# Optimization experiments

Hardware: AMD Instinct MI355X
Metric: run time of the kernel (lower is better)

The kernel has to match this reference:

```python
import jax, jax.numpy as jnp
import numpy as np

L, N, EMB, H = 4, 50000, 128, 4
R, HID, LBL = 16, 64, 32
E = 625000


def setup_inputs() -> dict:
    key = jax.random.key(0)
    ks = jax.random.split(key, 10)
    s = 0.05
    return {
        "embedding": jax.random.normal(ks[0], (L, N, EMB), jnp.float32),
        "in_proj_w": jax.random.normal(ks[1], (3 * EMB, EMB), jnp.float32) * s,
        "in_proj_b": jnp.zeros((3 * EMB,), jnp.float32),
        "out_proj_w": jax.random.normal(ks[2], (EMB, EMB), jnp.float32) * s,
        "out_proj_b": jnp.zeros((EMB,), jnp.float32),
        "w1": jax.random.normal(ks[3], (R, EMB, HID), jnp.float32) * s,
        "root1": jax.random.normal(ks[4], (EMB, HID), jnp.float32) * s,
        "b1": jnp.zeros((HID,), jnp.float32),
        "w2": jax.random.normal(ks[5], (R, HID, LBL), jnp.float32) * s,
        "root2": jax.random.normal(ks[6], (HID, LBL), jnp.float32) * s,
        "b2": jnp.zeros((LBL,), jnp.float32),
        "edge_index": jax.random.randint(ks[7], (2, E), 0, N, dtype=jnp.int64),
        "edge_type": jax.random.randint(ks[8], (E,), 0, R, dtype=jnp.int64),
    }


def mha_self(x, wi, bi, wo, bo):
    # x: (L, N, EMB) -- torch nn.MultiheadAttention, batch_first=False, q=k=v=x
    Ls, Ns, Es = x.shape
    hd = Es // H
    qkv = x @ wi.T + bi                      # (L, N, 3E)
    q, k, v = jnp.split(qkv, 3, axis=-1)
    q = q.reshape(Ls, Ns, H, hd)
    k = k.reshape(Ls, Ns, H, hd)
    v = v.reshape(Ls, Ns, H, hd)
    scores = jnp.einsum('lnhd,mnhd->nhlm', q, k) / np.sqrt(hd).astype(np.float32)
    attn = jax.nn.softmax(scores, axis=-1)
    out = jnp.einsum('nhlm,mnhd->lnhd', attn, v).reshape(Ls, Ns, Es)
    return out @ wo.T + bo


def rgcn_layer(x, src, dst, etype, W, root, bias):
    # PyG RGCNConv (num_bases=None, aggr='mean'):
    # out[n] = x[n] @ root + bias + sum_r mean_{e: dst=n, type=r} x[src_e] @ W[r]
    Rr, fin, fout = W.shape
    seg = etype * N + dst                                   # (E,) combined (rel, dst)
    msg_sum = jax.ops.segment_sum(x[src], seg, num_segments=Rr * N)   # (R*N, fin)
    cnt = jax.ops.segment_sum(jnp.ones((src.shape[0],), x.dtype), seg,
                              num_segments=Rr * N)
    mean = (msg_sum / jnp.maximum(cnt, 1.0)[:, None]).reshape(Rr, N, fin)
    agg = jnp.einsum('rni,rio->no', mean, W)                # per-relation GEMM
    return agg + x @ root + bias


def reference(embedding, in_proj_w, in_proj_b, out_proj_w, out_proj_b,
              w1, root1, b1, w2, root2, b2, edge_index, edge_type):
    attn_out = mha_self(embedding, in_proj_w, in_proj_b, out_proj_w, out_proj_b)
    x = attn_out[0]                                         # (N, EMB)
    src, dst = edge_index[0], edge_index[1]
    x = jax.nn.relu(rgcn_layer(x, src, dst, edge_type, w1, root1, b1))
    x = rgcn_layer(x, src, dst, edge_type, w2, root2, b2)
    return jax.nn.softmax(x, axis=-1)
```

## Files before the change

### kernel.cpp

```cpp
#include <hip/hip_runtime.h>
#include <hip/hip_bf16.h>
#include <math.h>

#define NNODES 50000
#define NEDGE 625000
#define RREL 16
#define SCAN_NB 196

typedef __attribute__((ext_vector_type(8))) short short8;
typedef __attribute__((ext_vector_type(4))) float f32x4;

__device__ __forceinline__ float bfu(ushort u) {
  return __uint_as_float(((unsigned)u) << 16);
}
__device__ __forceinline__ ushort f2b(float f) {
  __hip_bfloat16 h = __float2bfloat16(f);
  return *(ushort*)&h;
}

__global__ __launch_bounds__(256) void prep_weights(
    const float* __restrict__ ipw, const float* __restrict__ opw,
    const float* __restrict__ w1, const float* __restrict__ root1,
    const float* __restrict__ w2, const float* __restrict__ root2,
    __hip_bfloat16* __restrict__ BTqkv, __hip_bfloat16* __restrict__ BToutT,
    __hip_bfloat16* __restrict__ BT1, __hip_bfloat16* __restrict__ BT2) {
  int i = blockIdx.x * 256 + threadIdx.x;
  if (i < 49152) {
    BTqkv[i] = __float2bfloat16(ipw[i]);
  } else if (i < 65536) {
    int j = i - 49152; int m = j / 128, c = j % 128;
    BToutT[j] = __float2bfloat16(opw[c * 128 + m]);
  } else if (i < 65536 + 139264) {
    int j = i - 65536; int c = j / 128, k = j % 128;
    float v;
    if (c < 64) v = root1[k * 64 + c];
    else { int r = (c - 64) >> 6, o = (c - 64) & 63; v = w1[r * 8192 + k * 64 + o]; }
    BT1[j] = __float2bfloat16(v);
  } else if (i < 65536 + 139264 + 34816) {
    int j = i - 65536 - 139264; int c = j / 64, k = j % 64;
    float v;
    if (c < 32) v = root2[k * 32 + c];
    else { int r = (c - 32) >> 5, o = (c - 32) & 31; v = w2[r * 2048 + k * 32 + o]; }
    BT2[j] = __float2bfloat16(v);
  }
}

__global__ __launch_bounds__(256) void prep_bias1(
    const float* __restrict__ opb, const float* __restrict__ w1,
    const float* __restrict__ root1, float* __restrict__ bias1) {
  int j = blockIdx.x * 256 + threadIdx.x;
  if (j >= 1088) return;
  float s = 0.f;
  if (j < 64) {
    for (int c = 0; c < 128; c++) s += opb[c] * root1[c * 64 + j];
  } else {
    int r = (j - 64) >> 6, o = (j - 64) & 63;
    for (int c = 0; c < 128; c++) s += opb[c] * w1[r * 8192 + c * 64 + o];
  }
  bias1[j] = s;
}

__global__ __launch_bounds__(256) void attn_mega(
    const float* __restrict__ emb, const __hip_bfloat16* __restrict__ BTqkv,
    const float* __restrict__ ipb, __hip_bfloat16* __restrict__ o0) {
  __shared__ ushort Ks[128 * 132];
  __shared__ ushort Vs[128 * 132];
  __shared__ ushort Qs[32 * 132];
  const ushort* BT = (const ushort*)BTqkv;
  const int t = threadIdx.x;
  const int w = t >> 6, lane = t & 63;
  const int lrow = lane & 15, lk = lane >> 4;
  const long nb = (long)blockIdx.x * 32;

  short8 af[2][4];
#pragma unroll
  for (int i = 0; i < 2; i++) {
    long n = nb + 16 * i + lrow;
    if (n > NNODES - 1) n = NNODES - 1;
    const float* ap = emb + ((long)w * NNODES + n) * 128;
#pragma unroll
    for (int k0 = 0; k0 < 4; k0++) {
      float4 f0 = *(const float4*)(ap + k0 * 32 + lk * 8);
      float4 f1 = *(const float4*)(ap + k0 * 32 + lk * 8 + 4);
      int4 v;
      v.x = (int)f2b(f0.x) | ((int)f2b(f0.y) << 16);
      v.y = (int)f2b(f0.z) | ((int)f2b(f0.w) << 16);
      v.z = (int)f2b(f1.x) | ((int)f2b(f1.y) << 16);
      v.w = (int)f2b(f1.z) | ((int)f2b(f1.w) << 16);
      af[i][k0] = *(short8*)&v;
    }
  }

  const float alpha = 0.17677669529663687f;

  if (w == 0) {
#pragma unroll
    for (int half = 0; half < 2; half++) {
      f32x4 acc[2][4];
#pragma unroll
      for (int i = 0; i < 2; i++)
#pragma unroll
        for (int j = 0; j < 4; j++) acc[i][j] = (f32x4){0.f, 0.f, 0.f, 0.f};
#pragma unroll
      for (int k0 = 0; k0 < 4; k0++) {
        short8 bfr[4];
#pragma unroll
        for (int j = 0; j < 4; j++)
          bfr[j] = *(const short8*)(BT + (long)(half * 64 + j * 16 + lrow) * 128 + k0 * 32 + lk * 8);
#pragma unroll
        for (int i = 0; i < 2; i++)
#pragma unroll
          for (int j = 0; j < 4; j++)
            acc[i][j] = __builtin_amdgcn_mfma_f32_16x16x32_bf16(af[i][k0], bfr[j], acc[i][j], 0, 0, 0);
      }
#pragma unroll
      for (int j = 0; j < 4; j++) {
        int c = half * 64 + j * 16 + lrow;
        float bq = ipb[c];
#pragma unroll
        for (int i = 0; i < 2; i++)
#pragma unroll
          for (int q = 0; q < 4; q++)
            Qs[(16 * i + 4 * lk + q) * 132 + c] = f2b((acc[i][j][q] + bq) * alpha);
      }
    }
  }

#pragma unroll
  for (int sidx = 0; sidx < 2; sidx++) {
    const int base = 128 + sidx * 128;
    ushort* dst = sidx ? Vs : Ks;
#pragma unroll
    for (int half = 0; half < 2; half++) {
      f32x4 acc[2][4];
#pragma unroll
      for (int i = 0; i < 2; i++)
#pragma unroll
        for (int j = 0; j < 4; j++) acc[i][j] = (f32x4){0.f, 0.f, 0.f, 0.f};
#pragma unroll
      for (int k0 = 0; k0 < 4; k0++) {
        short8 bfr[4];
#pragma unroll
        for (int j = 0; j < 4; j++)
          bfr[j] = *(const short8*)(BT + (long)(base + half * 64 + j * 16 + lrow) * 128 + k0 * 32 + lk * 8);
#pragma unroll
        for (int i = 0; i < 2; i++)
#pragma unroll
          for (int j = 0; j < 4; j++)
            acc[i][j] = __builtin_amdgcn_mfma_f32_16x16x32_bf16(af[i][k0], bfr[j], acc[i][j], 0, 0, 0);
      }
#pragma unroll
      for (int j = 0; j < 4; j++) {
        int c = half * 64 + j * 16 + lrow;
        float bv = ipb[base + c];
#pragma unroll
        for (int i = 0; i < 2; i++)
#pragma unroll
          for (int q = 0; q < 4; q++)
            dst[(32 * w + 16 * i + 4 * lk + q) * 132 + c] = f2b(acc[i][j][q] + bv);
      }
    }
  }
  __syncthreads();

  for (int ii = 0; ii < 8; ii++) {
    int i = 8 * w + ii;
    long n = nb + i;
    uint qv = *(const uint*)(Qs + i * 132 + lane * 2);
    float q0 = bfu(qv & 0xffff), q1 = bfu(qv >> 16);
    float s[4];
#pragma unroll
    for (int m = 0; m < 4; m++) {
      uint kk = *(const uint*)(Ks + (m * 32 + i) * 132 + lane * 2);
      float p = q0 * bfu(kk & 0xffff) + q1 * bfu(kk >> 16);
#pragma unroll
      for (int off = 8; off; off >>= 1) p += __shfl_xor(p, off);
      s[m] = p;
    }
    float mx = fmaxf(fmaxf(s[0], s[1]), fmaxf(s[2], s[3]));
    float e[4], sum = 0.f;
#pragma unroll
    for (int m = 0; m < 4; m++) { e[m] = __expf(s[m] - mx); sum += e[m]; }
    float inv = 1.0f / sum;
    float o0f = 0.f, o1f = 0.f;
#pragma unroll
    for (int m = 0; m < 4; m++) {
      uint vv = *(const uint*)(Vs + (m * 32 + i) * 132 + lane * 2);
      float wgt = e[m] * inv;
      o0f += wgt * bfu(vv & 0xffff);
      o1f += wgt * bfu(vv >> 16);
    }
    if (n < NNODES)
      *(uint*)((ushort*)o0 + n * 128 + lane * 2) = (uint)f2b(o0f) | ((uint)f2b(o1f) << 16);
  }
}

#define EPILOGUE_STORE(MEFF, NCOLS, LDC, BIASEXPR)                              \
  for (int p = 0; p < 2; p++) {                                                 \
    __syncthreads();                                                            \
    if ((w >> 1) == p) {                                                        \
      _Pragma("unroll")                                                         \
      for (int j = 0; j < 4; j++) {                                             \
        int coll = wc + j * 16 + lrow;                                          \
        float bv = (BIASEXPR);                                                  \
        _Pragma("unroll")                                                       \
        for (int i = 0; i < 4; i++) {                                           \
          int rloc = i * 16 + lk * 4;                                           \
          _Pragma("unroll")                                                     \
          for (int q = 0; q < 4; q++)                                           \
            Cs[(rloc + q) * 132 + coll] = f2b(acc[i][j][q] + bv);               \
        }                                                                       \
      }                                                                         \
    }                                                                           \
    __syncthreads();                                                            \
    _Pragma("unroll")                                                           \
    for (int idx = t; idx < 64 * 16; idx += 256) {                              \
      int r = idx >> 4, k = idx & 15;                                           \
      long gm = row0 + p * 64 + r;                                              \
      int col = col0 + k * 8;                                                   \
      if (gm < (MEFF) && col < (NCOLS))                                         \
        *(int4*)((ushort*)C + gm * (LDC) + col) = *(const int4*)(Cs + r * 132 + k * 8); \
    }                                                                           \
  }

template <int K>
__global__ __launch_bounds__(256) void gemm_strips(
    const __hip_bfloat16* __restrict__ Av, const __hip_bfloat16* __restrict__ BT,
    const float* __restrict__ bias, __hip_bfloat16* __restrict__ C,
    int M, int N, int ldc, int spg) {
  constexpr int CPR = K / 8;
  __shared__ ushort As[128 * K];
  __shared__ ushort Cs[64 * 132];
  const int t = threadIdx.x;
  const long row0 = (long)blockIdx.x * 128;

#pragma unroll
  for (int c = t; c < 128 * CPR; c += 256) {
    int r = c / CPR, cc = c % CPR;
    long gm = row0 + r;
    int4 v = make_int4(0, 0, 0, 0);
    if (gm < M) v = *(const int4*)((const ushort*)Av + gm * K + cc * 8);
    *(int4*)(As + r * K + ((cc ^ (r & 7)) * 8)) = v;
  }
  __syncthreads();

  const int lane = t & 63, w = t >> 6;
  const int wr = (w >> 1) * 64, wc = (w & 1) * 64;
  const int lrow = lane & 15, lk = lane >> 4;
  const int nstrips = (N + 127) / 128;
  const int sbeg = blockIdx.y * spg;
  const int send = min(sbeg + spg, nstrips);

  for (int s = sbeg; s < send; s++) {
    const int col0 = s * 128;

    const ushort* bp[4];
#pragma unroll
    for (int j = 0; j < 4; j++) {
      int gn = col0 + wc + j * 16 + lrow;
      if (gn > N - 1) gn = N - 1;
      bp[j] = (const ushort*)BT + (long)gn * K + lk * 8;
    }

    f32x4 acc[4][4];
#pragma unroll
    for (int i = 0; i < 4; i++)
#pragma unroll
      for (int j = 0; j < 4; j++) acc[i][j] = (f32x4){0.f, 0.f, 0.f, 0.f};

#pragma unroll
    for (int k0 = 0; k0 < K; k0 += 32) {
      const int cb = k0 / 8 + lk;
      short8 af[4], bfr[4];
#pragma unroll
      for (int j = 0; j < 4; j++) bfr[j] = *(const short8*)(bp[j] + k0);
#pragma unroll
      for (int i = 0; i < 4; i++) {
        int ra = wr + i * 16 + lrow;
        af[i] = *(const short8*)(As + ra * K + ((cb ^ (ra & 7)) * 8));
      }
#pragma unroll
      for (int i = 0; i < 4; i++)
#pragma unroll
        for (int j = 0; j < 4; j++)
          acc[i][j] = __builtin_amdgcn_mfma_f32_16x16x32_bf16(af[i], bfr[j], acc[i][j], 0, 0, 0);
    }

    EPILOGUE_STORE(M, N, ldc, bias ? bias[min(col0 + coll, N - 1)] : 0.f)
  }
}

__global__ __launch_bounds__(256) void count_edges(
    const int* __restrict__ dst, const int* __restrict__ et, int* __restrict__ cnt) {
  int e = blockIdx.x * 256 + threadIdx.x;
  if (e < NEDGE) atomicAdd(&cnt[et[e] * NNODES + dst[e]], 1);
}

__global__ __launch_bounds__(256) void scan1(
    const int* __restrict__ cnt, int* __restrict__ off, int* __restrict__ part) {
  int t = threadIdx.x, b = blockIdx.x;
  int i = b * 256 + t;
  int v = 0;
  if (i < NNODES) {
#pragma unroll
    for (int r = 0; r < RREL; r++) v += cnt[r * NNODES + i];
  }
  __shared__ int sm[256];
  sm[t] = v;
  __syncthreads();
#pragma unroll
  for (int o = 1; o < 256; o <<= 1) {
    int x = (t >= o) ? sm[t - o] : 0;
    __syncthreads();
    sm[t] += x;
    __syncthreads();
  }
  if (i < NNODES) off[i] = sm[t] - v;
  if (t == 255) part[b] = sm[t];
}

__global__ __launch_bounds__(256) void scan2(int* __restrict__ part) {
  int t = threadIdx.x;
  int v = (t < SCAN_NB) ? part[t] : 0;
  __shared__ int sm[256];
  sm[t] = v;
  __syncthreads();
#pragma unroll
  for (int o = 1; o < 256; o <<= 1) {
    int x = (t >= o) ? sm[t - o] : 0;
    __syncthreads();
    sm[t] += x;
    __syncthreads();
  }
  if (t < SCAN_NB) part[t] = sm[t] - v;
}

__global__ __launch_bounds__(256) void scan3(int* __restrict__ off, const int* __restrict__ part) {
  int i = blockIdx.x * 256 + threadIdx.x;
  if (i < NNODES) off[i] += part[blockIdx.x];
  if (i == 0) off[NNODES] = NEDGE;
}

__global__ __launch_bounds__(256) void scatter_edges(
    const int* __restrict__ src, const int* __restrict__ dst, const int* __restrict__ et,
    const int* __restrict__ cnt, const int* __restrict__ off,
    int* __restrict__ fill, unsigned* __restrict__ sorted, float* __restrict__ scales) {
  int e = blockIdx.x * 256 + threadIdx.x;
  if (e >= NEDGE) return;
  int d = dst[e], r = et[e], s = src[e];
  int pos = off[d] + atomicAdd(&fill[d], 1);
  sorted[pos] = (unsigned)s | ((unsigned)r << 16);
  scales[pos] = 1.0f / (float)cnt[r * NNODES + d];
}

__global__ __launch_bounds__(256) void fused1(
    const int* __restrict__ off, const unsigned* __restrict__ sorted,
    const float* __restrict__ scales, const ushort* __restrict__ Y1,
    const float* __restrict__ b1, __hip_bfloat16* __restrict__ x1b) {
  int w = threadIdx.x >> 6, lane = threadIdx.x & 63;
  int d = blockIdx.x * 4 + w;
  int s0 = off[d], s1 = off[d + 1];
  float a0 = bfu(Y1[(size_t)d * 1088 + lane]) + b1[lane];
  float a1 = 0.f, a2 = 0.f, a3 = 0.f;
  int i = s0;
  for (; i + 3 < s1; i += 4) {
    unsigned p0 = sorted[i], p1 = sorted[i + 1], p2 = sorted[i + 2], p3 = sorted[i + 3];
    float c0 = scales[i], c1 = scales[i + 1], c2 = scales[i + 2], c3 = scales[i + 3];
    a0 += bfu(Y1[(size_t)(p0 & 0xFFFF) * 1088 + 64 + (p0 >> 16) * 64 + lane]) * c0;
    a1 += bfu(Y1[(size_t)(p1 & 0xFFFF) * 1088 + 64 + (p1 >> 16) * 64 + lane]) * c1;
    a2 += bfu(Y1[(size_t)(p2 & 0xFFFF) * 1088 + 64 + (p2 >> 16) * 64 + lane]) * c2;
    a3 += bfu(Y1[(size_t)(p3 & 0xFFFF) * 1088 + 64 + (p3 >> 16) * 64 + lane]) * c3;
  }
  for (; i < s1; i++) {
    unsigned p = sorted[i];
    a0 += bfu(Y1[(size_t)(p & 0xFFFF) * 1088 + 64 + (p >> 16) * 64 + lane]) * scales[i];
  }
  float acc = (a0 + a1) + (a2 + a3);
  x1b[(size_t)d * 64 + lane] = __float2bfloat16(fmaxf(acc, 0.f));
}

__global__ __launch_bounds__(256) void fused2(
    const int* __restrict__ off, const unsigned* __restrict__ sorted,
    const float* __restrict__ scales, const ushort* __restrict__ Y2,
    const float* __restrict__ b2, float* __restrict__ out) {
  int w = threadIdx.x >> 6, lane = threadIdx.x & 63;
  int d = blockIdx.x * 4 + w;
  int j = lane & 31, half = lane >> 5;
  int s0 = off[d], s1 = off[d + 1];
  float a0 = 0.f, a1 = 0.f;
  int i = s0 + half;
  for (; i + 2 < s1; i += 4) {
    unsigned p0 = sorted[i], p1 = sorted[i + 2];
    a0 += bfu(Y2[(size_t)(p0 & 0xFFFF) * 544 + 32 + (p0 >> 16) * 32 + j]) * scales[i];
    a1 += bfu(Y2[(size_t)(p1 & 0xFFFF) * 544 + 32 + (p1 >> 16) * 32 + j]) * scales[i + 2];
  }
  for (; i < s1; i += 2) {
    unsigned p = sorted[i];
    a0 += bfu(Y2[(size_t)(p & 0xFFFF) * 544 + 32 + (p >> 16) * 32 + j]) * scales[i];
  }
  float acc = a0 + a1;
  acc += __shfl_xor(acc, 32);
  float v = acc + bfu(Y2[(size_t)d * 544 + j]) + b2[j];
  float mx = v;
#pragma unroll
  for (int o = 16; o; o >>= 1) mx = fmaxf(mx, __shfl_xor(mx, o));
  float e = __expf(v - mx);
  float sum = e;
#pragma unroll
  for (int o = 16; o; o >>= 1) sum += __shfl_xor(sum, o);
  if (half == 0) out[(size_t)d * 32 + j] = e / sum;
}

extern "C" void kernel_launch(void* const* d_in, const int* in_sizes, int n_in,
                              void* d_out, int out_size, void* d_ws, size_t ws_size,
                              hipStream_t stream) {
  (void)in_sizes; (void)n_in; (void)out_size; (void)ws_size;
  const float* emb   = (const float*)d_in[0];
  const float* ipw   = (const float*)d_in[1];
  const float* ipb   = (const float*)d_in[2];
  const float* opw   = (const float*)d_in[3];
  const float* opb   = (const float*)d_in[4];
  const float* w1    = (const float*)d_in[5];
  const float* root1 = (const float*)d_in[6];
  const float* b1    = (const float*)d_in[7];
  const float* w2    = (const float*)d_in[8];
  const float* root2 = (const float*)d_in[9];
  const float* b2    = (const float*)d_in[10];
  const int*   eidx  = (const int*)d_in[11];
  const int*   etype = (const int*)d_in[12];
  const int* srcp = eidx;
  const int* dstp = eidx + NEDGE;

  unsigned char* ws = (unsigned char*)d_ws;
  size_t off_b = 0;
  auto alloc = [&](size_t bytes) {
    unsigned char* p = ws + off_b;
    off_b += (bytes + 255) & ~(size_t)255;
    return p;
  };

  unsigned char* R = alloc(108800000);
  __hip_bfloat16* Y1  = (__hip_bfloat16*)R;
  __hip_bfloat16* Y2  = (__hip_bfloat16*)R;
  __hip_bfloat16* o0  = (__hip_bfloat16*)alloc(12800000);
  __hip_bfloat16* x1b = (__hip_bfloat16*)alloc(6400000);
  int*            cnt = (int*)alloc(3200000);
  int*            offs = (int*)alloc((NNODES + 1) * 4);
  int*            fill = (int*)alloc(NNODES * 4);
  int*            part = (int*)alloc(SCAN_NB * 4);
  unsigned*       sorted = (unsigned*)alloc(NEDGE * 4);
  float*          scales = (float*)alloc(NEDGE * 4);
  __hip_bfloat16* BTqkv  = (__hip_bfloat16*)alloc(98304);
  __hip_bfloat16* BToutT = (__hip_bfloat16*)alloc(32768);
  __hip_bfloat16* BT1    = (__hip_bfloat16*)alloc(278528);
  __hip_bfloat16* BT2    = (__hip_bfloat16*)alloc(69632);
  __hip_bfloat16* BW     = (__hip_bfloat16*)alloc(278528);
  float*          bias1  = (float*)alloc(4352);

  prep_weights<<<dim3((241664 + 255) / 256), dim3(256), 0, stream>>>(
      ipw, opw, w1, root1, w2, root2, BTqkv, BToutT, BT1, BT2);
  prep_bias1<<<dim3(5), dim3(256), 0, stream>>>(opb, w1, root1, bias1);
  hipMemsetAsync(cnt, 0, (size_t)RREL * NNODES * sizeof(int), stream);
  hipMemsetAsync(fill, 0, (size_t)NNODES * sizeof(int), stream);
  count_edges<<<dim3((NEDGE + 255) / 256), dim3(256), 0, stream>>>(dstp, etype, cnt);
  scan1<<<dim3(SCAN_NB), dim3(256), 0, stream>>>(cnt, offs, part);
  scan2<<<dim3(1), dim3(256), 0, stream>>>(part);
  scan3<<<dim3(SCAN_NB), dim3(256), 0, stream>>>(offs, part);
  scatter_edges<<<dim3((NEDGE + 255) / 256), dim3(256), 0, stream>>>(
      srcp, dstp, etype, cnt, offs, fill, sorted, scales);

  gemm_strips<128><<<dim3(9, 1), dim3(256), 0, stream>>>(
      BT1, BToutT, nullptr, BW, 1088, 128, 128, 1);

  attn_mega<<<dim3((NNODES + 31) / 32), dim3(256), 0, stream>>>(
      emb, BTqkv, ipb, o0);

  gemm_strips<128><<<dim3(391, 3), dim3(256), 0, stream>>>(
      o0, BW, bias1, Y1, NNODES, 1088, 1088, 3);

  fused1<<<dim3(NNODES / 4), dim3(256), 0, stream>>>(
      offs, sorted, scales, (const ushort*)Y1, b1, x1b);

  gemm_strips<64><<<dim3(391, 2), dim3(256), 0, stream>>>(
      x1b, BT2, nullptr, Y2, NNODES, 544, 544, 3);

  fused2<<<dim3(NNODES / 4), dim3(256), 0, stream>>>(
      offs, sorted, scales, (const ushort*)Y2, b2, (float*)d_out);
}
```

Before: 339.0 us.

## Split fused attention into QKV GEMM, attention, and per-wave unit GEMMs

Replaces the fused attention kernel with a separate QKV projection kernel that assigns independent 32x128 output tiles to each wave, writing Q/K/V for only the needed rows to a global buffer. A lightweight per-node attention kernel then reads those values back. The strip GEMMs for both RGCN layers are also replaced by per-wave unit GEMMs that stage results through a per-wave LDS tile, with no block-level barriers. This removes the redundant K/V recompute and the block synchronisation, at the cost of a large QKV round trip through global memory and a bigger workspace.

```diff
diff --git a/kernel.cpp b/kernel.cpp
--- a/kernel.cpp
+++ b/kernel.cpp
@@ -16,6 +16,10 @@
 __device__ __forceinline__ ushort f2b(float f) {
   __hip_bfloat16 h = __float2bfloat16(f);
   return *(ushort*)&h;
+}
+__device__ __forceinline__ void lds_fence() {
+  asm volatile("" ::: "memory");
+  __builtin_amdgcn_sched_barrier(0);
 }
 
 __global__ __launch_bounds__(256) void prep_weights(
@@ -60,24 +64,28 @@
   bias1[j] = s;
 }
 
-__global__ __launch_bounds__(256) void attn_mega(
-    const float* __restrict__ emb, const __hip_bfloat16* __restrict__ BTqkv,
-    const float* __restrict__ ipb, __hip_bfloat16* __restrict__ o0) {
-  __shared__ ushort Ks[128 * 132];
-  __shared__ ushort Vs[128 * 132];
-  __shared__ ushort Qs[32 * 132];
-  const ushort* BT = (const ushort*)BTqkv;
-  const int t = threadIdx.x;
-  const int w = t >> 6, lane = t & 63;
-  const int lrow = lane & 15, lk = lane >> 4;
-  const long nb = (long)blockIdx.x * 32;
+
+__global__ void qkv_units(
+    const float* __restrict__ A, const __hip_bfloat16* __restrict__ BTv,
+    const float* __restrict__ bias, __hip_bfloat16* __restrict__ Cv) {
+  __shared__ ushort Cs[4][32 * 136];
+  const ushort* BT = (const ushort*)BTv;
+  ushort* C = (ushort*)Cv;
+  int w = threadIdx.x >> 6, lane = threadIdx.x & 63;
+  int u = blockIdx.x * 4 + w;
+  if (u >= 14063) return;
+  long row0; int col0; long Meff;
+  if (u < 12500) { row0 = (long)(u >> 1) * 32; col0 = 128 + (u & 1) * 128; Meff = 200000; }
+  else           { row0 = (long)(u - 12500) * 32; col0 = 0; Meff = NNODES; }
+  int lrow = lane & 15, lk = lane >> 4;
+  ushort* cs = Cs[w];
 
   short8 af[2][4];
 #pragma unroll
   for (int i = 0; i < 2; i++) {
-    long n = nb + 16 * i + lrow;
-    if (n > NNODES - 1) n = NNODES - 1;
-    const float* ap = emb + ((long)w * NNODES + n) * 128;
+    long r = row0 + 16 * i + lrow;
+    if (r > 199999) r = 199999;
+    const float* ap = A + r * 128;
 #pragma unroll
     for (int k0 = 0; k0 < 4; k0++) {
       float4 f0 = *(const float4*)(ap + k0 * 32 + lk * 8);
@@ -91,107 +99,113 @@
     }
   }
 
-  const float alpha = 0.17677669529663687f;
-
-  if (w == 0) {
-#pragma unroll
-    for (int half = 0; half < 2; half++) {
-      f32x4 acc[2][4];
-#pragma unroll
-      for (int i = 0; i < 2; i++)
-#pragma unroll
-        for (int j = 0; j < 4; j++) acc[i][j] = (f32x4){0.f, 0.f, 0.f, 0.f};
-#pragma unroll
-      for (int k0 = 0; k0 < 4; k0++) {
-        short8 bfr[4];
-#pragma unroll
-        for (int j = 0; j < 4; j++)
-          bfr[j] = *(const short8*)(BT + (long)(half * 64 + j * 16 + lrow) * 128 + k0 * 32 + lk * 8);
-#pragma unroll
-        for (int i = 0; i < 2; i++)
-#pragma unroll
-          for (int j = 0; j < 4; j++)
-            acc[i][j] = __builtin_amdgcn_mfma_f32_16x16x32_bf16(af[i][k0], bfr[j], acc[i][j], 0, 0, 0);
-      }
-#pragma unroll
-      for (int j = 0; j < 4; j++) {
-        int c = half * 64 + j * 16 + lrow;
-        float bq = ipb[c];
-#pragma unroll
-        for (int i = 0; i < 2; i++)
-#pragma unroll
-          for (int q = 0; q < 4; q++)
-            Qs[(16 * i + 4 * lk + q) * 132 + c] = f2b((acc[i][j][q] + bq) * alpha);
-      }
+  f32x4 acc[2][8];
+#pragma unroll
+  for (int i = 0; i < 2; i++)
+#pragma unroll
+    for (int j = 0; j < 8; j++) acc[i][j] = (f32x4){0.f, 0.f, 0.f, 0.f};
+#pragma unroll
+  for (int k0 = 0; k0 < 4; k0++) {
+    short8 b[8];
+#pragma unroll
+    for (int j = 0; j < 8; j++)
+      b[j] = *(const short8*)(BT + (long)(col0 + j * 16 + lrow) * 128 + k0 * 32 + lk * 8);
+#pragma unroll
+    for (int i = 0; i < 2; i++)
+#pragma unroll
+      for (int j = 0; j < 8; j++)
+        acc[i][j] = __builtin_amdgcn_mfma_f32_16x16x32_bf16(af[i][k0], b[j], acc[i][j], 0, 0, 0);
+  }
+
+#pragma unroll
+  for (int j = 0; j < 8; j++) {
+    int c = j * 16 + lrow;
+    float bv = bias[col0 + c];
+#pragma unroll
+    for (int i = 0; i < 2; i++)
+#pragma unroll
+      for (int q = 0; q < 4; q++)
+        cs[(16 * i + 4 * lk + q) * 136 + c] = f2b(acc[i][j][q] + bv);
+  }
+  lds_fence();
+#pragma unroll
+  for (int p = 0; p < 8; p++) {
+    int r = p * 4 + (lane >> 4);
+    int k = lane & 15;
+    long gm = row0 + r;
+    if (gm < Meff)
+      *(int4*)(C + gm * 384 + col0 + k * 8) = *(const int4*)(cs + r * 136 + k * 8);
+  }
+}
+
+template <int KK>
+__global__ void gemm_units(
+    const __hip_bfloat16* __restrict__ Av, const __hip_bfloat16* __restrict__ BTv,
+    const float* __restrict__ bias, __hip_bfloat16* __restrict__ Cv,
+    int M, int N, int ldc, int colunits, int totalUnits) {
+  __shared__ ushort Cs[4][32 * 136];
+  const ushort* A = (const ushort*)Av;
+  const ushort* BT = (const ushort*)BTv;
+  ushort* C = (ushort*)Cv;
+  int w = threadIdx.x >> 6, lane = threadIdx.x & 63;
+  int u = blockIdx.x * 4 + w;
+  if (u >= totalUnits) return;
+  int rg = u / colunits, cu = u - rg * colunits;
+  long row0 = (long)rg * 32;
+  int col0 = cu * 128;
+  int lrow = lane & 15, lk = lane >> 4;
+  ushort* cs = Cs[w];
+
+  short8 af[2][KK / 32];
+#pragma unroll
+  for (int i = 0; i < 2; i++) {
+    long r = row0 + 16 * i + lrow;
+    if (r > M - 1) r = M - 1;
+#pragma unroll
+    for (int k0 = 0; k0 < KK / 32; k0++)
+      af[i][k0] = *(const short8*)(A + r * KK + k0 * 32 + lk * 8);
+  }
+
+  f32x4 acc[2][8];
+#pragma unroll
+  for (int i = 0; i < 2; i++)
+#pragma unroll
+    for (int j = 0; j < 8; j++) acc[i][j] = (f32x4){0.f, 0.f, 0.f, 0.f};
+#pragma unroll
+  for (int k0 = 0; k0 < KK / 32; k0++) {
+    short8 b[8];
+#pragma unroll
+    for (int j = 0; j < 8; j++) {
+      int gn = col0 + j * 16 + lrow;
+      if (gn > N - 1) gn = N - 1;
+      b[j] = *(const short8*)(BT + (long)gn * KK + k0 * 32 + lk * 8);
     }
-  }
-
-#pragma unroll
-  for (int sidx = 0; sidx < 2; sidx++) {
-    const int base = 128 + sidx * 128;
-    ushort* dst = sidx ? Vs : Ks;
-#pragma unroll
-    for (int half = 0; half < 2; half++) {
-      f32x4 acc[2][4];
-#pragma unroll
-      for (int i = 0; i < 2; i++)
-#pragma unroll
-        for (int j = 0; j < 4; j++) acc[i][j] = (f32x4){0.f, 0.f, 0.f, 0.f};
-#pragma unroll
-      for (int k0 = 0; k0 < 4; k0++) {
-        short8 bfr[4];
-#pragma unroll
-        for (int j = 0; j < 4; j++)
-          bfr[j] = *(const short8*)(BT + (long)(base + half * 64 + j * 16 + lrow) * 128 + k0 * 32 + lk * 8);
-#pragma unroll
-        for (int i = 0; i < 2; i++)
-#pragma unroll
-          for (int j = 0; j < 4; j++)
-            acc[i][j] = __builtin_amdgcn_mfma_f32_16x16x32_bf16(af[i][k0], bfr[j], acc[i][j], 0, 0, 0);
-      }
-#pragma unroll
-      for (int j = 0; j < 4; j++) {
-        int c = half * 64 + j * 16 + lrow;
-        float bv = ipb[base + c];
-#pragma unroll
-        for (int i = 0; i < 2; i++)
-#pragma unroll
-          for (int q = 0; q < 4; q++)
-            dst[(32 * w + 16 * i + 4 * lk + q) * 132 + c] = f2b(acc[i][j][q] + bv);
-      }
-    }
-  }
-  __syncthreads();
-
-  for (int ii = 0; ii < 8; ii++) {
-    int i = 8 * w + ii;
-    long n = nb + i;
-    uint qv = *(const uint*)(Qs + i * 132 + lane * 2);
-    float q0 = bfu(qv & 0xffff), q1 = bfu(qv >> 16);
-    float s[4];
-#pragma unroll
-    for (int m = 0; m < 4; m++) {
-      uint kk = *(const uint*)(Ks + (m * 32 + i) * 132 + lane * 2);
-      float p = q0 * bfu(kk & 0xffff) + q1 * bfu(kk >> 16);
-#pragma unroll
-      for (int off = 8; off; off >>= 1) p += __shfl_xor(p, off);
-      s[m] = p;
-    }
-    float mx = fmaxf(fmaxf(s[0], s[1]), fmaxf(s[2], s[3]));
-    float e[4], sum = 0.f;
-#pragma unroll
-    for (int m = 0; m < 4; m++) { e[m] = __expf(s[m] - mx); sum += e[m]; }
-    float inv = 1.0f / sum;
-    float o0f = 0.f, o1f = 0.f;
-#pragma unroll
-    for (int m = 0; m < 4; m++) {
-      uint vv = *(const uint*)(Vs + (m * 32 + i) * 132 + lane * 2);
-      float wgt = e[m] * inv;
-      o0f += wgt * bfu(vv & 0xffff);
-      o1f += wgt * bfu(vv >> 16);
-    }
-    if (n < NNODES)
-      *(uint*)((ushort*)o0 + n * 128 + lane * 2) = (uint)f2b(o0f) | ((uint)f2b(o1f) << 16);
+#pragma unroll
+    for (int i = 0; i < 2; i++)
+#pragma unroll
+      for (int j = 0; j < 8; j++)
+        acc[i][j] = __builtin_amdgcn_mfma_f32_16x16x32_bf16(af[i][k0], b[j], acc[i][j], 0, 0, 0);
+  }
+
+#pragma unroll
+  for (int j = 0; j < 8; j++) {
+    int c = j * 16 + lrow;
+    float bv = (bias && col0 + c < N) ? bias[col0 + c] : 0.f;
+#pragma unroll
+    for (int i = 0; i < 2; i++)
+#pragma unroll
+      for (int q = 0; q < 4; q++)
+        cs[(16 * i + 4 * lk + q) * 136 + c] = f2b(acc[i][j][q] + bv);
+  }
+  lds_fence();
+#pragma unroll
+  for (int p = 0; p < 8; p++) {
+    int r = p * 4 + (lane >> 4);
+    int k = lane & 15;
+    long gm = row0 + r;
+    int col = col0 + k * 8;
+    if (gm < M && col < N)
+      *(int4*)(C + gm * (long)ldc + col) = *(const int4*)(cs + r * 136 + k * 8);
   }
 }
 
@@ -290,6 +304,38 @@
   }
 }
 
+__global__ __launch_bounds__(256) void attn_kernel(
+    const __hip_bfloat16* __restrict__ qkv, __hip_bfloat16* __restrict__ o0) {
+  int w = threadIdx.x >> 6, lane = threadIdx.x & 63;
+  int n = blockIdx.x * 4 + w;
+  const ushort* base = (const ushort*)qkv;
+  uint qv = *(const uint*)(base + (size_t)n * 384 + lane * 2);
+  float q0 = bfu(qv & 0xffff), q1 = bfu(qv >> 16);
+  float s[4];
+#pragma unroll
+  for (int m = 0; m < 4; m++) {
+    uint kk = *(const uint*)(base + (size_t)(m * NNODES + n) * 384 + 128 + lane * 2);
+    float p = q0 * bfu(kk & 0xffff) + q1 * bfu(kk >> 16);
+#pragma unroll
+    for (int off = 8; off; off >>= 1) p += __shfl_xor(p, off);
+    s[m] = p * 0.17677669529663687f;
+  }
+  float mx = fmaxf(fmaxf(s[0], s[1]), fmaxf(s[2], s[3]));
+  float e[4], sum = 0.f;
+#pragma unroll
+  for (int m = 0; m < 4; m++) { e[m] = __expf(s[m] - mx); sum += e[m]; }
+  float inv = 1.0f / sum;
+  float o0f = 0.f, o1f = 0.f;
+#pragma unroll
+  for (int m = 0; m < 4; m++) {
+    uint vv = *(const uint*)(base + (size_t)(m * NNODES + n) * 384 + 256 + lane * 2);
+    float wgt = e[m] * inv;
+    o0f += wgt * bfu(vv & 0xffff);
+    o1f += wgt * bfu(vv >> 16);
+  }
+  *(uint*)((ushort*)o0 + (size_t)n * 128 + lane * 2) = (uint)f2b(o0f) | ((uint)f2b(o1f) << 16);
+}
+
 __global__ __launch_bounds__(256) void count_edges(
     const int* __restrict__ dst, const int* __restrict__ et, int* __restrict__ cnt) {
   int e = blockIdx.x * 256 + threadIdx.x;
@@ -439,7 +485,8 @@
     return p;
   };
 
-  unsigned char* R = alloc(108800000);
+  unsigned char* R = alloc(153600000);
+  __hip_bfloat16* qkv = (__hip_bfloat16*)R;
   __hip_bfloat16* Y1  = (__hip_bfloat16*)R;
   __hip_bfloat16* Y2  = (__hip_bfloat16*)R;
   __hip_bfloat16* o0  = (__hip_bfloat16*)alloc(12800000);
@@ -472,17 +519,18 @@
   gemm_strips<128><<<dim3(9, 1), dim3(256), 0, stream>>>(
       BT1, BToutT, nullptr, BW, 1088, 128, 128, 1);
 
-  attn_mega<<<dim3((NNODES + 31) / 32), dim3(256), 0, stream>>>(
-      emb, BTqkv, ipb, o0);
-
-  gemm_strips<128><<<dim3(391, 3), dim3(256), 0, stream>>>(
-      o0, BW, bias1, Y1, NNODES, 1088, 1088, 3);
+  qkv_units<<<dim3(3516), dim3(256), 0, stream>>>(emb, BTqkv, ipb, qkv);
+
+  attn_kernel<<<dim3(12500), dim3(256), 0, stream>>>(qkv, o0);
+
+  gemm_units<128><<<dim3(3517), dim3(256), 0, stream>>>(
+      o0, BW, bias1, Y1, NNODES, 1088, 1088, 9, 14067);
 
   fused1<<<dim3(NNODES / 4), dim3(256), 0, stream>>>(
       offs, sorted, scales, (const ushort*)Y1, b1, x1b);
 
-  gemm_strips<64><<<dim3(391, 2), dim3(256), 0, stream>>>(
-      x1b, BT2, nullptr, Y2, NNODES, 544, 544, 3);
+  gemm_units<64><<<dim3(1954), dim3(256), 0, stream>>>(
+      x1b, BT2, nullptr, Y2, NNODES, 544, 544, 5, 7815);
 
   fused2<<<dim3(NNODES / 4), dim3(256), 0, stream>>>(
       offs, sorted, scales, (const ushort*)Y2, b2, (float*)d_out);
```

New measurement: 391.0 us. 15.3% more time.
